# Kernel optimization log

Measured on AMD Instinct MI355X. Metric: run time of the kernel, lower is better.

Reference implementation:

```python
import jax, jax.numpy as jnp
import numpy as np

N = 4096      # num_nodes
B = 32        # batch_size
DIN, DH, DOUT = 64, 128, 32
DIM = 40      # GraphCons embedding dim (hard-coded in source)
ALPHA = 3.0


def setup_inputs() -> dict:
    key = jax.random.key(0)
    ks = jax.random.split(key, 11)
    p = lambda k, shape: (jax.random.normal(k, shape, dtype=jnp.float32) * 0.05)
    return {
        "x": jax.random.normal(ks[0], (B * N, DIN), dtype=jnp.float32),
        "emb1": p(ks[1], (N, DIM)),
        "emb2": p(ks[2], (N, DIM)),
        "lin1_w": p(ks[3], (DIM, DIM)),
        "lin1_b": p(ks[4], (DIM,)),
        "lin2_w": p(ks[5], (DIM, DIM)),
        "lin2_b": p(ks[6], (DIM,)),
        "gcn1_w": p(ks[7], (DIN, DH)),
        "gcn1_b": p(ks[8], (DH,)),
        "gcn2_w": p(ks[9], (DH, DOUT)),
        "gcn2_b": p(ks[10], (DOUT,)),
    }


def reference(x, emb1, emb2, lin1_w, lin1_b, lin2_w, lin2_b,
              gcn1_w, gcn1_b, gcn2_w, gcn2_b):
    # --- GraphCons: learned adjacency. idx = arange(N) so emb(idx) == table.
    n1 = jnp.tanh(ALPHA * (emb1 @ lin1_w + lin1_b))          # [N, DIM]
    n2 = jnp.tanh(ALPHA * (emb2 @ lin2_w + lin2_b))          # [N, DIM]
    a = n1 @ n2.T - n2 @ n1.T                                # [N, N] antisymmetric
    adj = jax.nn.relu(jnp.tanh(ALPHA * a))
    # k == N, so topk/scatter mask is all-ones: adjacency structure = nonzero(adj).
    A = (adj > 0).astype(jnp.float32)                        # binary, zero diagonal
    M = A + jnp.eye(N, dtype=jnp.float32)                    # add self-loops
    # GCN symmetric norm: deg over destination (column) nodes.
    dinv = jax.lax.rsqrt(jnp.sum(M, axis=0))                 # [N], deg >= 1
    Ahat = M * (dinv[:, None] * dinv[None, :])               # [N, N]
    # Batched block-diagonal graph: B independent copies sharing Ahat.
    xb = x.astype(jnp.float32).reshape(B, N, DIN)
    # out[j] = sum_i Ahat[i, j] * (X W)[i]  -> contract over source i
    h = jnp.einsum('ij,bif->bjf', Ahat, xb @ gcn1_w) + gcn1_b  # [B, N, DH]
    h = jax.nn.relu(h)
    h = jnp.einsum('ij,bif->bjf', Ahat, h @ gcn2_w) + gcn2_b   # [B, N, DOUT]
    out = jax.nn.softmax(h, axis=-1)
    return out.reshape(B * N, DOUT)
```

## Files before the change

kernel.cpp:

```cpp
#include <hip/hip_runtime.h>

typedef float f32x4 __attribute__((ext_vector_type(4)));
typedef short s16x8 __attribute__((ext_vector_type(8)));
typedef short s16x4 __attribute__((ext_vector_type(4)));
typedef int i32x4 __attribute__((ext_vector_type(4)));

#define NN 4096
#define NB 32
#define DIN 64
#define DH 128
#define DOUT 32
#define DIM 40
#define KADJ 512

__device__ __forceinline__ unsigned short f2bf(float f) {
    unsigned int u = __float_as_uint(f);
    unsigned int r = (u + 0x7FFFu + ((u >> 16) & 1u)) >> 16;
    return (unsigned short)r;
}
__device__ __forceinline__ float bf2f(unsigned short h) {
    return __uint_as_float(((unsigned int)h) << 16);
}
__device__ __forceinline__ void gload16(const void* g, void* l) {
    __builtin_amdgcn_global_load_lds(
        (const __attribute__((address_space(1))) unsigned int*)g,
        (__attribute__((address_space(3))) unsigned int*)l, 16, 0, 0);
}
__device__ __forceinline__ void bar() {
    asm volatile("" ::: "memory");
    __builtin_amdgcn_s_barrier();
    asm volatile("" ::: "memory");
}

__global__ __launch_bounds__(256) void k_embuv(
    const float* __restrict__ emb1, const float* __restrict__ emb2,
    const float* __restrict__ l1w, const float* __restrict__ l1b,
    const float* __restrict__ l2w, const float* __restrict__ l2b,
    unsigned short* __restrict__ Ux, unsigned short* __restrict__ Vx,
    int* __restrict__ deg)
{
    __shared__ float e1s[16 * DIM], e2s[16 * DIM];
    __shared__ float w1s[DIM * DIM], w2s[DIM * DIM], b1s[DIM], b2s[DIM];
    __shared__ unsigned short Ul[16][KADJ], Vl[16][KADJ];
    const int tid = threadIdx.x;
    const int node0 = blockIdx.x * 16;
    if (tid < 16) deg[node0 + tid] = 0;
    for (int i = tid; i < 16 * DIM; i += 256) {
        e1s[i] = emb1[node0 * DIM + i];
        e2s[i] = emb2[node0 * DIM + i];
    }
    for (int i = tid; i < DIM * DIM; i += 256) { w1s[i] = l1w[i]; w2s[i] = l2w[i]; }
    if (tid < DIM) { b1s[tid] = l1b[tid]; b2s[tid] = l2b[tid]; }
    __syncthreads();
    const int r = tid >> 4;
    const int k0 = (tid & 15) * 5;
    const int PMAP[6] = {0, 0, 1, 1, 0, 2};
    const int QMAP[6] = {0, 1, 0, 1, 2, 0};
    #pragma unroll
    for (int e = 0; e < 5; e++) {
        int k = k0 + e;
        int kp = (k < DIM) ? k : k - DIM;
        float acc1 = b1s[kp], acc2 = b2s[kp];
        for (int kk = 0; kk < DIM; kk++) {
            acc1 += e1s[r * DIM + kk] * w1s[kk * DIM + kp];
            acc2 += e2s[r * DIM + kk] * w2s[kk * DIM + kp];
        }
        float n1v = tanhf(3.0f * acc1), n2v = tanhf(3.0f * acc2);
        float a = (k < DIM) ? n1v : -n2v;
        float b = (k < DIM) ? n2v : n1v;
        unsigned short u0 = f2bf(a); float ra = a - bf2f(u0);
        unsigned short u1 = f2bf(ra); ra -= bf2f(u1);
        unsigned short u2 = f2bf(ra);
        unsigned short v0 = f2bf(b); float rb = b - bf2f(v0);
        unsigned short v1 = f2bf(rb); rb -= bf2f(v1);
        unsigned short v2 = f2bf(rb);
        unsigned short uu[3] = {u0, u1, u2}, vv[3] = {v0, v1, v2};
        #pragma unroll
        for (int bq = 0; bq < 6; bq++) {
            Ul[r][80 * bq + k] = uu[PMAP[bq]];
            Vl[r][80 * bq + k] = vv[QMAP[bq]];
        }
    }
    {
        int c = tid & 15;
        Ul[r][480 + c * 2]     = 0; Vl[r][480 + c * 2]     = 0;
        Ul[r][480 + c * 2 + 1] = 0; Vl[r][480 + c * 2 + 1] = 0;
    }
    __syncthreads();
    #pragma unroll
    for (int q = 0; q < 4; q++) {
        int idx = q * 256 + tid;
        int rr = idx >> 6, c8 = idx & 63;
        size_t off = ((size_t)(node0 + rr)) * KADJ + c8 * 8;
        *(s16x8*)(Ux + off) = *(s16x8*)&Ul[rr][c8 * 8];
        *(s16x8*)(Vx + off) = *(s16x8*)&Vl[rr][c8 * 8];
    }
}

__global__ __launch_bounds__(512, 2) void gemm_adj8(
    const unsigned short* __restrict__ A, const unsigned short* __restrict__ Bt,
    char* __restrict__ Mi8, int* __restrict__ deg)
{
    constexpr int K = KADJ;
    constexpr int NT = K / 64;
    __shared__ __align__(16) unsigned short As[2][256 * 64];
    __shared__ __align__(16) unsigned short Bs[2][256 * 64];

    const int tid = threadIdx.x;
    const int lane = tid & 63;
    const int w = tid >> 6;
    const int wm = w >> 2, wn = w & 3;
    const int fr = lane & 15, kg = lane >> 4;

    const int bid = blockIdx.x;
    const int swz = (bid & 7) * 32 + (bid >> 3);
    const int bx = swz & 15, by = swz >> 4;
    const int c0 = bx * 256, j0 = by * 256;

    const int cid0 = w * 128 + lane, cid1 = cid0 + 64;
    const int r0 = cid0 >> 3, k0c = cid0 & 7;
    const int r1 = cid1 >> 3, k1c = cid1 & 7;
    const int so0 = r0 * K + ((k0c ^ (r0 & 7)) << 3);
    const int so1 = r1 * K + ((k1c ^ (r1 & 7)) << 3);
    const int lb0 = (w * 2 + 0) * 512;
    const int lb1 = (w * 2 + 1) * 512;

    const unsigned short* Aj = A + (size_t)j0 * K;
    const unsigned short* Bc = Bt + (size_t)c0 * K;

#define STAGE_A(buf, half, kt) do { \
    const unsigned short* g_ = Aj + (size_t)((half) * 128) * K + (kt); \
    gload16(g_ + so0, &As[buf][(half) * 8192 + lb0]); \
    gload16(g_ + so1, &As[buf][(half) * 8192 + lb1]); } while (0)
#define STAGE_B(buf, half, kt) do { \
    const unsigned short* g_ = Bc + (size_t)((half) * 128) * K + (kt); \
    gload16(g_ + so0, &Bs[buf][(half) * 8192 + lb0]); \
    gload16(g_ + so1, &Bs[buf][(half) * 8192 + lb1]); } while (0)

    STAGE_A(0, 0, 0);  STAGE_A(0, 1, 0);
    STAGE_B(0, 0, 0);  STAGE_B(0, 1, 0);
    STAGE_A(1, 0, 64); STAGE_A(1, 1, 64);
    STAGE_B(1, 0, 64);
    asm volatile("s_waitcnt vmcnt(6)" ::: "memory");
    bar();

    const int x0 = ((kg) ^ (fr & 7)) << 4;
    const int x1 = ((4 + kg) ^ (fr & 7)) << 4;
    int aOff[8], bOff[4];
    #pragma unroll
    for (int m = 0; m < 8; m++) aOff[m] = (wm * 128 + m * 16 + fr) * 128;
    #pragma unroll
    for (int n = 0; n < 4; n++) bOff[n] = (wn * 64 + n * 16 + fr) * 128;

    s16x8 af0c[4], bf0c[4];
    #pragma unroll
    for (int m = 0; m < 4; m++) af0c[m] = *(const s16x8*)((const char*)As[0] + aOff[m] + x0);
    #pragma unroll
    for (int n = 0; n < 4; n++) bf0c[n] = *(const s16x8*)((const char*)Bs[0] + bOff[n] + x0);

    f32x4 acc[8][4] = {};

    for (int t = 0; t < NT; t++) {
        const int P = t & 1;
        const char* Ap = (const char*)As[P];
        const char* Bp = (const char*)Bs[P];
        const char* Aq = (const char*)As[P ^ 1];
        const char* Bq = (const char*)Bs[P ^ 1];
        const int kt1 = (t + 1) * 64, kt2 = (t + 2) * 64;
        const bool s1 = (t + 1) < NT, s2 = (t + 2) < NT;
        s16x8 af0h[4], af1l[4], af1h[4], bf1[4], af0n[4], bf0n[4];

        #pragma unroll
        for (int m = 0; m < 4; m++) af0h[m] = *(const s16x8*)(Ap + aOff[m + 4] + x0);
        #pragma unroll
        for (int m = 0; m < 4; m++) af1l[m] = *(const s16x8*)(Ap + aOff[m] + x1);
        if (s1) STAGE_B(P ^ 1, 1, kt1);
        __builtin_amdgcn_s_setprio(1);
        #pragma unroll
        for (int m = 0; m < 4; m++)
            #pragma unroll
            for (int n = 0; n < 4; n++)
                acc[m][n] = __builtin_amdgcn_mfma_f32_16x16x32_bf16(af0c[m], bf0c[n], acc[m][n], 0, 0, 0);
        __builtin_amdgcn_s_setprio(0);

        #pragma unroll
        for (int m = 0; m < 4; m++) af1h[m] = *(const s16x8*)(Ap + aOff[m + 4] + x1);
        #pragma unroll
        for (int n = 0; n < 4; n++) bf1[n] = *(const s16x8*)(Bp + bOff[n] + x1);
        __builtin_amdgcn_s_setprio(1);
        #pragma unroll
        for (int m = 4; m < 8; m++)
            #pragma unroll
            for (int n = 0; n < 4; n++)
                acc[m][n] = __builtin_amdgcn_mfma_f32_16x16x32_bf16(af0h[m - 4], bf0c[n], acc[m][n], 0, 0, 0);
        __builtin_amdgcn_s_setprio(0);
        asm volatile("s_waitcnt lgkmcnt(0)" ::: "memory");
        bar();

        __builtin_amdgcn_s_setprio(1);
        #pragma unroll
        for (int m = 0; m < 4; m++)
            #pragma unroll
            for (int n = 0; n < 4; n++)
                acc[m][n] = __builtin_amdgcn_mfma_f32_16x16x32_bf16(af1l[m], bf1[n], acc[m][n], 0, 0, 0);
        __builtin_amdgcn_s_setprio(0);
        if (s2) {
            STAGE_A(P, 0, kt2);
            STAGE_A(P, 1, kt2);
            STAGE_B(P, 0, kt2);
            asm volatile("s_waitcnt vmcnt(6)" ::: "memory");
        } else {
            asm volatile("s_waitcnt vmcnt(0)" ::: "memory");
        }
        bar();

        if (s1) {
            #pragma unroll
            for (int m = 0; m < 4; m++) af0n[m] = *(const s16x8*)(Aq + aOff[m] + x0);
            #pragma unroll
            for (int n = 0; n < 4; n++) bf0n[n] = *(const s16x8*)(Bq + bOff[n] + x0);
        }
        __builtin_amdgcn_s_setprio(1);
        #pragma unroll
        for (int m = 4; m < 8; m++)
            #pragma unroll
            for (int n = 0; n < 4; n++)
                acc[m][n] = __builtin_amdgcn_mfma_f32_16x16x32_bf16(af1h[m - 4], bf1[n], acc[m][n], 0, 0, 0);
        __builtin_amdgcn_s_setprio(0);
        if (s1) {
            #pragma unroll
            for (int m = 0; m < 4; m++) af0c[m] = af0n[m];
            #pragma unroll
            for (int n = 0; n < 4; n++) bf0c[n] = bf0n[n];
        }
    }
#undef STAGE_A
#undef STAGE_B

    #pragma unroll
    for (int m = 0; m < 8; m++) {
        int rbase = j0 + wm * 128 + m * 16 + kg * 4;
        #pragma unroll
        for (int r = 0; r < 4; r++) {
            int row = rbase + r;
            int cnt = 0;
            #pragma unroll
            for (int n = 0; n < 4; n++) {
                int col = c0 + wn * 64 + n * 16 + fr;
                bool bit = (acc[m][n][r] > 0.f) || (row == col);
                Mi8[(size_t)row * NN + col] = bit ? (char)1 : (char)0;
                cnt += bit ? 1 : 0;
            }
            cnt += __shfl_xor(cnt, 1);
            cnt += __shfl_xor(cnt, 2);
            cnt += __shfl_xor(cnt, 4);
            cnt += __shfl_xor(cnt, 8);
            if (fr == 0) atomicAdd(&deg[row], cnt);
        }
    }
}

__global__ void k_dinv(const int* __restrict__ deg, float* __restrict__ dinv,
                       unsigned int* __restrict__ smY) {
    int i = blockIdx.x * 256 + threadIdx.x;
    if (i < NN) { dinv[i] = 1.0f / sqrtf((float)deg[i]); smY[i] = 0u; }
}

__global__ __launch_bounds__(256) void k_y1m(
    const float* __restrict__ x, const float* __restrict__ W1,
    const float* __restrict__ dinv, unsigned short* __restrict__ YT,
    unsigned int* __restrict__ smY)
{
    __shared__ __align__(16) unsigned short Xs[128 * 64];
    __shared__ __align__(16) unsigned short Ws[128 * 64];
    const int tid = threadIdx.x;
    const int i0 = blockIdx.x * 128, b = blockIdx.y;

    const float* xg = x + ((size_t)(b * NN + i0)) * DIN;
    #pragma unroll
    for (int q = 0; q < 8; q++) {
        int idx = q * 256 + tid;
        int row = idx >> 4, c4 = idx & 15;
        f32x4 v = *(const f32x4*)(xg + (size_t)row * DIN + c4 * 4);
        s16x4 pk;
        #pragma unroll
        for (int e = 0; e < 4; e++) pk[e] = (short)f2bf(v[e]);
        int chunk = (c4 >> 1) ^ (row & 7);
        *(s16x4*)((char*)Xs + row * 128 + (chunk << 4) + (c4 & 1) * 8) = pk;
    }
    #pragma unroll
    for (int q = 0; q < 8; q++) {
        int idx = q * 256 + tid;
        int k = idx >> 5, f4 = (idx & 31) * 4;
        f32x4 v = ((const f32x4*)W1)[idx];
        #pragma unroll
        for (int e = 0; e < 4; e++) {
            int f = f4 + e;
            int chunk = (k >> 3) ^ (f & 7);
            *(unsigned short*)((char*)Ws + f * 128 + (chunk << 4) + (k & 7) * 2) = f2bf(v[e]);
        }
    }
    __syncthreads();

    const int lane = tid & 63, w = tid >> 6;
    const int wm = w >> 1, wn = w & 1;
    const int fr = lane & 15, kg = lane >> 4;
    f32x4 acc[4][4] = {};
    #pragma unroll
    for (int ks = 0; ks < 2; ks++) {
        int kc = ks * 4 + kg;
        s16x8 af[4], bf[4];
        #pragma unroll
        for (int mt = 0; mt < 4; mt++) {
            int row = wm * 64 + mt * 16 + fr;
            af[mt] = *(const s16x8*)((const char*)Xs + row * 128 + ((kc ^ (row & 7)) << 4));
        }
        #pragma unroll
        for (int nt = 0; nt < 4; nt++) {
            int f = wn * 64 + nt * 16 + fr;
            bf[nt] = *(const s16x8*)((const char*)Ws + f * 128 + ((kc ^ (f & 7)) << 4));
        }
        #pragma unroll
        for (int mt = 0; mt < 4; mt++)
            #pragma unroll
            for (int nt = 0; nt < 4; nt++)
                acc[mt][nt] = __builtin_amdgcn_mfma_f32_16x16x32_bf16(af[mt], bf[nt], acc[mt][nt], 0, 0, 0);
    }
    float am[4] = {0.f, 0.f, 0.f, 0.f};
    #pragma unroll
    for (int mt = 0; mt < 4; mt++) {
        int ibase = i0 + wm * 64 + mt * 16 + kg * 4;
        float dv[4];
        #pragma unroll
        for (int r = 0; r < 4; r++) dv[r] = dinv[ibase + r];
        #pragma unroll
        for (int nt = 0; nt < 4; nt++) {
            int f = wn * 64 + nt * 16 + fr;
            s16x4 pk;
            #pragma unroll
            for (int r = 0; r < 4; r++) {
                float v = acc[mt][nt][r] * dv[r];
                am[nt] = fmaxf(am[nt], fabsf(v));
                pk[r] = (short)f2bf(v);
            }
            *(s16x4*)(YT + (size_t)(b * DH + f) * NN + ibase) = pk;
        }
    }
    #pragma unroll
    for (int nt = 0; nt < 4; nt++) {
        float mv = am[nt];
        mv = fmaxf(mv, __shfl_xor(mv, 16));
        mv = fmaxf(mv, __shfl_xor(mv, 32));
        if (kg == 0)
            atomicMax(&smY[b * DH + wn * 64 + nt * 16 + fr], __float_as_uint(mv));
    }
}

__global__ __launch_bounds__(256) void k_quant(
    const unsigned short* __restrict__ src, const unsigned int* __restrict__ smax,
    char* __restrict__ dst)
{
    const int c = blockIdx.x;
    const float s = __uint_as_float(smax[c]);
    const float inv = s > 0.f ? 127.0f / s : 0.f;
    const unsigned short* row = src + (size_t)c * NN;
    char* orow = dst + (size_t)c * NN;
    const int base = threadIdx.x * 16;
    s16x8 a = *(const s16x8*)(row + base);
    s16x8 b = *(const s16x8*)(row + base + 8);
    union { char c8[16]; i32x4 v; } u;
    #pragma unroll
    for (int e = 0; e < 8; e++) {
        int q = (int)rintf(bf2f((unsigned short)a[e]) * inv);
        q = q > 127 ? 127 : (q < -127 ? -127 : q);
        u.c8[e] = (char)q;
    }
    #pragma unroll
    for (int e = 0; e < 8; e++) {
        int q = (int)rintf(bf2f((unsigned short)b[e]) * inv);
        q = q > 127 ? 127 : (q < -127 ? -127 : q);
        u.c8[8 + e] = (char)q;
    }
    *(i32x4*)(orow + base) = u.v;
}

__global__ __launch_bounds__(512, 2) void gemm8qi(
    const char* __restrict__ A, const char* __restrict__ Bt,
    unsigned short* __restrict__ H, const float* __restrict__ dinv,
    const unsigned int* __restrict__ smY, const float* __restrict__ bias)
{
    constexpr int KB = NN;
    constexpr int NT = 32;
    __shared__ __align__(16) char As[2][256 * 128];
    __shared__ __align__(16) char Bs[2][256 * 128];

    const int tid = threadIdx.x;
    const int lane = tid & 63;
    const int w = tid >> 6;
    const int wm = w >> 2, wn = w & 3;
    const int fr = lane & 15, kg = lane >> 4;

    const int bid = blockIdx.x;
    const int swz = (bid & 7) * 32 + (bid >> 3);
    const int bx = swz & 15, by = swz >> 4;
    const int c0 = bx * 256, j0 = by * 256;

    const char* Aj = A + (size_t)j0 * KB;
    const char* Bc = Bt + (size_t)c0 * KB;

    const int lr = tid >> 3, kcs = tid & 7;

#define STAGE_AQ(buf, q, kt) do { \
    int ra_ = (q) * 64 + lr; \
    int rb_ = ra_ + 128; \
    gload16(Aj + (size_t)ra_ * KB + (kt) + ((kcs ^ (ra_ & 7)) << 4), \
            &As[buf][(q) * 8192 + tid * 16]); \
    gload16(Aj + (size_t)rb_ * KB + (kt) + ((kcs ^ (rb_ & 7)) << 4), \
            &As[buf][(q) * 8192 + 16384 + tid * 16]); \
} while (0)
#define STAGE_BQ(buf, nh, kt) do { \
    int ca_ = tid, cb_ = tid + 512; \
    int r0_ = (ca_ >> 8) * 64 + (nh) * 32 + ((ca_ >> 3) & 31); \
    int r1_ = (cb_ >> 8) * 64 + (nh) * 32 + ((cb_ >> 3) & 31); \
    gload16(Bc + (size_t)r0_ * KB + (kt) + (((ca_ & 7) ^ (r0_ & 7)) << 4), \
            &Bs[buf][(ca_ >> 8) * 8192 + (nh) * 4096 + (ca_ & 255) * 16]); \
    gload16(Bc + (size_t)r1_ * KB + (kt) + (((cb_ & 7) ^ (r1_ & 7)) << 4), \
            &Bs[buf][(cb_ >> 8) * 8192 + (nh) * 4096 + (cb_ & 255) * 16]); \
} while (0)

    STAGE_AQ(0, 0, 0); STAGE_AQ(0, 1, 0);
    STAGE_BQ(0, 0, 0); STAGE_BQ(0, 1, 0);
    STAGE_BQ(1, 0, 128); STAGE_BQ(1, 1, 128);
    asm volatile("s_waitcnt vmcnt(4)" ::: "memory");
    bar();

    const int x0 = ((kg) ^ (fr & 7)) << 4;
    const int x1 = ((4 + kg) ^ (fr & 7)) << 4;
    int aOff[8], bOff[4];
    #pragma unroll
    for (int m = 0; m < 8; m++) aOff[m] = (wm * 128 + m * 16 + fr) * 128;
    #pragma unroll
    for (int n = 0; n < 4; n++) bOff[n] = (wn * 64 + n * 16 + fr) * 128;

    i32x4 acc[8][4] = {};
    const char* A0p = (const char*)As[0];
    const char* B0p = (const char*)Bs[0];
    const char* A1p = (const char*)As[1];
    const char* B1p = (const char*)Bs[1];

#define MFMA_Q(MB, NB_, AF0, AF1, BK0, BK1) do { \
    __builtin_amdgcn_s_setprio(1); \
    _Pragma("unroll") \
    for (int m = 0; m < 4; m++) { \
        _Pragma("unroll") \
        for (int n = 0; n < 2; n++) { \
            acc[(MB) + m][(NB_) + n] = __builtin_amdgcn_mfma_i32_16x16x64_i8( \
                AF0[m], BK0[n], acc[(MB) + m][(NB_) + n], 0, 0, 0); \
            acc[(MB) + m][(NB_) + n] = __builtin_amdgcn_mfma_i32_16x16x64_i8( \
                AF1[m], BK1[n], acc[(MB) + m][(NB_) + n], 0, 0, 0); \
        } \
    } \
    __builtin_amdgcn_s_setprio(0); \
} while (0)

    i32x4 af0[4], af1[4], b0k0[2], b0k1[2], b1k0[2], b1k1[2];

    for (int T = 0; T < NT; T += 2) {
        const bool s2 = (T + 2) < NT, s3 = (T + 3) < NT;
        const int kt1 = (T + 1) * 128, kt2 = (T + 2) * 128, kt3 = (T + 3) * 128;

        #pragma unroll
        for (int m = 0; m < 4; m++) { af0[m] = *(const i32x4*)(A0p + aOff[m] + x0);
                                      af1[m] = *(const i32x4*)(A0p + aOff[m] + x1); }
        #pragma unroll
        for (int n = 0; n < 2; n++) { b0k0[n] = *(const i32x4*)(B0p + bOff[n] + x0);
                                      b0k1[n] = *(const i32x4*)(B0p + bOff[n] + x1); }
        STAGE_AQ(1, 0, kt1);
        bar();
        MFMA_Q(0, 0, af0, af1, b0k0, b0k1);
        bar();

        #pragma unroll
        for (int n = 0; n < 2; n++) { b1k0[n] = *(const i32x4*)(B0p + bOff[n + 2] + x0);
                                      b1k1[n] = *(const i32x4*)(B0p + bOff[n + 2] + x1); }
        STAGE_AQ(1, 1, kt1);
        bar();
        MFMA_Q(0, 2, af0, af1, b1k0, b1k1);
        bar();

        #pragma unroll
        for (int m = 0; m < 4; m++) { af0[m] = *(const i32x4*)(A0p + aOff[m + 4] + x0);
                                      af1[m] = *(const i32x4*)(A0p + aOff[m + 4] + x1); }
        if (s2) STAGE_BQ(0, 0, kt2);
        bar();
        MFMA_Q(4, 0, af0, af1, b0k0, b0k1);
        bar();

        if (s2) { STAGE_BQ(0, 1, kt2);
                  asm volatile("s_waitcnt vmcnt(4)" ::: "memory"); }
        else    { asm volatile("s_waitcnt vmcnt(0)" ::: "memory"); }
        bar();
        MFMA_Q(4, 2, af0, af1, b1k0, b1k1);
        bar();

        #pragma unroll
        for (int m = 0; m < 4; m++) { af0[m] = *(const i32x4*)(A1p + aOff[m] + x0);
                                      af1[m] = *(const i32x4*)(A1p + aOff[m] + x1); }
        #pragma unroll
        for (int n = 0; n < 2; n++) { b0k0[n] = *(const i32x4*)(B1p + bOff[n] + x0);
                                      b0k1[n] = *(const i32x4*)(B1p + bOff[n] + x1); }
        if (s2) STAGE_AQ(0, 0, kt2);
        bar();
        MFMA_Q(0, 0, af0, af1, b0k0, b0k1);
        bar();

        #pragma unroll
        for (int n = 0; n < 2; n++) { b1k0[n] = *(const i32x4*)(B1p + bOff[n + 2] + x0);
                                      b1k1[n] = *(const i32x4*)(B1p + bOff[n + 2] + x1); }
        if (s2) STAGE_AQ(0, 1, kt2);
        bar();
        MFMA_Q(0, 2, af0, af1, b1k0, b1k1);
        bar();

        #pragma unroll
        for (int m = 0; m < 4; m++) { af0[m] = *(const i32x4*)(A1p + aOff[m + 4] + x0);
                                      af1[m] = *(const i32x4*)(A1p + aOff[m + 4] + x1); }
        if (s3) STAGE_BQ(1, 0, kt3);
        bar();
        MFMA_Q(4, 0, af0, af1, b0k0, b0k1);
        bar();

        if (s3) { STAGE_BQ(1, 1, kt3);
                  asm volatile("s_waitcnt vmcnt(4)" ::: "memory"); }
        else    { asm volatile("s_waitcnt vmcnt(0)" ::: "memory"); }
        bar();
        MFMA_Q(4, 2, af0, af1, b1k0, b1k1);
        bar();
    }
#undef MFMA_Q
#undef STAGE_AQ
#undef STAGE_BQ

    #pragma unroll
    for (int m = 0; m < 8; m++) {
        int rbase = j0 + wm * 128 + m * 16 + kg * 4;
        float dv[4];
        #pragma unroll
        for (int r = 0; r < 4; r++) dv[r] = dinv[rbase + r];
        #pragma unroll
        for (int n = 0; n < 4; n++) {
            int gcol = c0 + wn * 64 + n * 16 + fr;
            float bb = bias[gcol & (DH - 1)];
            float sc = __uint_as_float(smY[gcol]) * (1.0f / 127.0f);
            #pragma unroll
            for (int r = 0; r < 4; r++) {
                float v = (float)acc[m][n][r] * sc * dv[r] + bb;
                v = v > 0.f ? v : 0.f;
                H[(size_t)(rbase + r) * NN + gcol] = f2bf(v);
            }
        }
    }
}

__global__ __launch_bounds__(256) void k_z2(
    const unsigned short* __restrict__ H, const float* __restrict__ W2,
    const float* __restrict__ dinv, unsigned short* __restrict__ ZT)
{
    __shared__ __align__(16) unsigned short Hs[128 * DH];
    __shared__ __align__(16) unsigned short W2Ts[DOUT * DH];
    const int tid = threadIdx.x;
    const int j0 = blockIdx.x * 128, b = blockIdx.y;
    const unsigned short* Hb = H + (size_t)j0 * NN + b * DH;

    #pragma unroll
    for (int q = 0; q < 8; q++) {
        int cid = q * 256 + tid;
        int row = cid >> 4, kc = cid & 15;
        gload16(Hb + (size_t)row * NN + kc * 8, &Hs[cid * 8]);
    }
    #pragma unroll
    for (int q = 0; q < 16; q++) {
        int idx = q * 256 + tid;
        int f = idx >> 5, g = idx & 31;
        W2Ts[g * DH + f] = f2bf(W2[f * DOUT + g]);
    }
    __syncthreads();

    const int lane = tid & 63, w = tid >> 6;
    const int fr = lane & 15, kg = lane >> 4;
    f32x4 acc[2][2] = {};
    #pragma unroll
    for (int ks = 0; ks < 4; ks++) {
        s16x8 af[2], bf[2];
        #pragma unroll
        for (int mt = 0; mt < 2; mt++) {
            int row = w * 32 + mt * 16 + fr;
            af[mt] = *(const s16x8*)&Hs[row * DH + ks * 32 + kg * 8];
        }
        #pragma unroll
        for (int nt = 0; nt < 2; nt++) {
            int g = nt * 16 + fr;
            bf[nt] = *(const s16x8*)&W2Ts[g * DH + ks * 32 + kg * 8];
        }
        #pragma unroll
        for (int mt = 0; mt < 2; mt++)
            #pragma unroll
            for (int nt = 0; nt < 2; nt++)
                acc[mt][nt] = __builtin_amdgcn_mfma_f32_16x16x32_bf16(af[mt], bf[nt], acc[mt][nt], 0, 0, 0);
    }
    #pragma unroll
    for (int mt = 0; mt < 2; mt++) {
        int jbase = j0 + w * 32 + mt * 16 + kg * 4;
        float dv[4];
        #pragma unroll
        for (int r = 0; r < 4; r++) dv[r] = dinv[jbase + r];
        #pragma unroll
        for (int nt = 0; nt < 2; nt++) {
            int g = nt * 16 + fr;
            s16x4 pk;
            #pragma unroll
            for (int r = 0; r < 4; r++)
                pk[r] = (short)f2bf(acc[mt][nt][r] * dv[r]);
            *(s16x4*)(ZT + (size_t)(b * DOUT + g) * NN + jbase) = pk;
        }
    }
}

__global__ __launch_bounds__(256) void gsm2h(
    const char* __restrict__ Mi8, const unsigned short* __restrict__ Bt,
    float* __restrict__ out, const float* __restrict__ dinv,
    const float* __restrict__ bias)
{
    constexpr int KB = NN;
    constexpr int K = NN;
    constexpr int NT = K / 64;
    __shared__ __align__(16) char AsmI[2][64 * 64];
    __shared__ __align__(16) unsigned short Bsm[2][128 * 64];
    const int tid = threadIdx.x;
    const int lane = tid & 63;
    const int w = tid >> 6;
    const int wm = w >> 1, wn = w & 1;
    const int c0 = blockIdx.x * 128;
    const int j0 = blockIdx.y * 64;
    const int fr = lane & 15, kg = lane >> 4;

    const int rowA = tid >> 2, kcA = tid & 3;
    const int srcA = rowA * KB + ((kcA ^ (rowA & 3)) << 4);
    int srcB[4];
    #pragma unroll
    for (int q = 0; q < 4; q++) {
        int cid = q * 256 + tid;
        int row = cid >> 3, kc = cid & 7;
        srcB[q] = row * K + ((kc ^ (row & 7)) << 3);
    }
    const char* Abase = Mi8 + (size_t)j0 * KB;
    const unsigned short* Bbase = Bt + (size_t)c0 * K;

#define STAGE_T(buf, kt) do { \
    gload16(Abase + (kt) + srcA, &AsmI[buf][tid * 16]); \
    _Pragma("unroll") \
    for (int q = 0; q < 4; q++) \
        gload16(Bbase + (kt) + srcB[q], &Bsm[buf][(q * 256 + tid) * 8]); } while (0)

    STAGE_T(0, 0);
    STAGE_T(1, 64);
    asm volatile("s_waitcnt vmcnt(5)" ::: "memory");
    bar();

    const int x0 = (kg ^ (fr & 7)) << 4;
    const int x1 = ((4 + kg) ^ (fr & 7)) << 4;
    int aRow[2], bOff[4];
    #pragma unroll
    for (int m = 0; m < 2; m++) aRow[m] = wm * 32 + m * 16 + fr;
    #pragma unroll
    for (int n = 0; n < 4; n++) bOff[n] = (wn * 64 + n * 16 + fr) * 128;

#define LOAD_AM(dst, Abuf, m_, ks_) do { \
    int kc_ = (ks_) * 2 + (kg >> 1); \
    const char* p_ = (Abuf) + aRow[m_] * 64 + ((kc_ ^ (aRow[m_] & 3)) << 4) + (kg & 1) * 8; \
    int v0_ = *(const int*)p_; \
    int v1_ = *(const int*)(p_ + 4); \
    _Pragma("unroll") \
    for (int e_ = 0; e_ < 4; e_++) dst[e_]     = ((v0_ >> (8 * e_)) & 0xFF) ? (short)0x3F80 : (short)0; \
    _Pragma("unroll") \
    for (int e_ = 0; e_ < 4; e_++) dst[4 + e_] = ((v1_ >> (8 * e_)) & 0xFF) ? (short)0x3F80 : (short)0; \
} while (0)

    s16x8 afc[2][2], bfc[2][4];
    #pragma unroll
    for (int ks = 0; ks < 2; ks++) {
        int xk = ks ? x1 : x0;
        #pragma unroll
        for (int m = 0; m < 2; m++) LOAD_AM(afc[ks][m], (const char*)AsmI[0], m, ks);
        #pragma unroll
        for (int n = 0; n < 4; n++) bfc[ks][n] = *(const s16x8*)((const char*)Bsm[0] + bOff[n] + xk);
    }
    asm volatile("s_waitcnt lgkmcnt(0)" ::: "memory");
    bar();

    f32x4 acc[2][4] = {};

    for (int t = 0; t < NT; t++) {
        const int P = t & 1;
        const bool s1 = (t + 1) < NT, s2 = (t + 2) < NT;

        if (s2) STAGE_T(P, (t + 2) * 64);
        __builtin_amdgcn_s_setprio(1);
        #pragma unroll
        for (int m = 0; m < 2; m++)
            #pragma unroll
            for (int n = 0; n < 4; n++)
                acc[m][n] = __builtin_amdgcn_mfma_f32_16x16x32_bf16(afc[0][m], bfc[0][n], acc[m][n], 0, 0, 0);
        __builtin_amdgcn_s_setprio(0);
        if (s2) asm volatile("s_waitcnt vmcnt(5)" ::: "memory");
        else    asm volatile("s_waitcnt vmcnt(0)" ::: "memory");
        bar();

        s16x8 afn[2][2], bfn[2][4];
        if (s1) {
            const char* Aq = (const char*)AsmI[P ^ 1];
            const char* Bq = (const char*)Bsm[P ^ 1];
            #pragma unroll
            for (int ks = 0; ks < 2; ks++) {
                int xk = ks ? x1 : x0;
                #pragma unroll
                for (int m = 0; m < 2; m++) LOAD_AM(afn[ks][m], Aq, m, ks);
                #pragma unroll
                for (int n = 0; n < 4; n++) bfn[ks][n] = *(const s16x8*)(Bq + bOff[n] + xk);
            }
        }
        __builtin_amdgcn_s_setprio(1);
        #pragma unroll
        for (int m = 0; m < 2; m++)
            #pragma unroll
            for (int n = 0; n < 4; n++)
                acc[m][n] = __builtin_amdgcn_mfma_f32_16x16x32_bf16(afc[1][m], bfc[1][n], acc[m][n], 0, 0, 0);
        __builtin_amdgcn_s_setprio(0);
        asm volatile("s_waitcnt lgkmcnt(0)" ::: "memory");
        bar();
        if (s1) {
            #pragma unroll
            for (int ks = 0; ks < 2; ks++) {
                #pragma unroll
                for (int m = 0; m < 2; m++) afc[ks][m] = afn[ks][m];
                #pragma unroll
                for (int n = 0; n < 4; n++) bfc[ks][n] = bfn[ks][n];
            }
        }
    }
#undef STAGE_T
#undef LOAD_AM

    const float b_lo = bias[fr], b_hi = bias[fr + 16];
    #pragma unroll
    for (int m = 0; m < 2; m++) {
        int rbase = j0 + wm * 32 + m * 16 + kg * 4;
        float dv[4];
        #pragma unroll
        for (int r = 0; r < 4; r++) dv[r] = dinv[rbase + r];
        #pragma unroll
        for (int np = 0; np < 2; np++) {
            int bg = (c0 >> 5) + wn * 2 + np;
            #pragma unroll
            for (int r = 0; r < 4; r++) {
                int row = rbase + r;
                float v0 = acc[m][np * 2][r]     * dv[r] + b_lo;
                float v1 = acc[m][np * 2 + 1][r] * dv[r] + b_hi;
                float mx = fmaxf(v0, v1);
                #pragma unroll
                for (int d = 8; d; d >>= 1) mx = fmaxf(mx, __shfl_xor(mx, d));
                float e0 = expf(v0 - mx), e1 = expf(v1 - mx);
                float s = e0 + e1;
                #pragma unroll
                for (int d = 8; d; d >>= 1) s += __shfl_xor(s, d);
                float inv = 1.0f / s;
                size_t ob = ((size_t)bg * NN + row) * DOUT;
                out[ob + fr]      = e0 * inv;
                out[ob + fr + 16] = e1 * inv;
            }
        }
    }
}

extern "C" void kernel_launch(void* const* d_in, const int* in_sizes, int n_in,
                              void* d_out, int out_size, void* d_ws, size_t ws_size,
                              hipStream_t stream)
{
    (void)in_sizes; (void)n_in; (void)out_size; (void)ws_size;
    const float* x    = (const float*)d_in[0];
    const float* emb1 = (const float*)d_in[1];
    const float* emb2 = (const float*)d_in[2];
    const float* l1w  = (const float*)d_in[3];
    const float* l1b  = (const float*)d_in[4];
    const float* l2w  = (const float*)d_in[5];
    const float* l2b  = (const float*)d_in[6];
    const float* g1w  = (const float*)d_in[7];
    const float* g1b  = (const float*)d_in[8];
    const float* g2w  = (const float*)d_in[9];
    const float* g2b  = (const float*)d_in[10];
    float* out = (float*)d_out;

    char* w = (char*)d_ws;
    int* deg = (int*)w;                       w += NN * 4;
    float* dinv = (float*)w;                  w += NN * 4;
    unsigned int* smY = (unsigned int*)w;     w += NN * 4;
    char* Mi8 = (char*)w;                     w += (size_t)NN * NN;
    unsigned short* YT = (unsigned short*)w;  w += (size_t)NN * NN * 2;
    char* Yq = (char*)w;                      w += (size_t)NN * NN;
    unsigned short* H  = (unsigned short*)w;  w += (size_t)NN * NN * 2;
    unsigned short* ZT = (unsigned short*)w;  w += (size_t)(NB * DOUT) * NN * 2;
    unsigned short* Ux = YT;
    unsigned short* Vx = YT + (size_t)NN * KADJ;

    k_embuv<<<256, 256, 0, stream>>>(emb1, emb2, l1w, l1b, l2w, l2b, Ux, Vx, deg);
    gemm_adj8<<<256, 512, 0, stream>>>(Vx, Ux, Mi8, deg);
    k_dinv<<<16, 256, 0, stream>>>(deg, dinv, smY);
    k_y1m<<<dim3(32, 32), 256, 0, stream>>>(x, g1w, dinv, YT, smY);
    k_quant<<<NN, 256, 0, stream>>>(YT, smY, Yq);
    gemm8qi<<<256, 512, 0, stream>>>(Mi8, Yq, H, dinv, smY, g1b);
    k_z2<<<dim3(32, 32), 256, 0, stream>>>(H, g2w, dinv, ZT);
    gsm2h<<<dim3(8, 64), 256, 0, stream>>>(Mi8, ZT, out, dinv, g2b);
}
```

Before: 224.6 us.

## Replace bf16 second aggregation GEMM with split int8 hi/lo quantized MFMA

The second propagation GEMM stops expanding the int8 adjacency into bf16 and multiplying with bf16 Z. Z is now quantized per column into two int8 planes (high part plus a scaled residual), and the kernel runs two i8 MFMAs per tile against the raw int8 adjacency, with 128-wide K steps. This removes the per-element byte-to-bf16 expansion and halves the B-operand bytes per plane, in exchange for an extra quantization kernel, an atomic max reduction in k_z2, and double the MFMA count. Accuracy depends on the two-level int8 representation matching bf16 closely enough.

After: 206.0 us. -8.3%, faster.

```diff
diff --git a/kernel.cpp b/kernel.cpp
--- a/kernel.cpp
+++ b/kernel.cpp
@@ -261,9 +261,10 @@
 }
 
 __global__ void k_dinv(const int* __restrict__ deg, float* __restrict__ dinv,
-                       unsigned int* __restrict__ smY) {
+                       unsigned int* __restrict__ smY, unsigned int* __restrict__ smZ) {
     int i = blockIdx.x * 256 + threadIdx.x;
     if (i < NN) { dinv[i] = 1.0f / sqrtf((float)deg[i]); smY[i] = 0u; }
+    if (i < NB * DOUT) smZ[i] = 0u;
 }
 
 __global__ __launch_bounds__(256) void k_y1m(
@@ -382,6 +383,33 @@
         u.c8[8 + e] = (char)q;
     }
     *(i32x4*)(orow + base) = u.v;
+}
+
+__global__ __launch_bounds__(256) void k_quant2(
+    const unsigned short* __restrict__ src, const unsigned int* __restrict__ smax,
+    char* __restrict__ dst)
+{
+    const int c = blockIdx.x;
+    const float s = __uint_as_float(smax[c]);
+    const float inv = s > 0.f ? 127.0f / s : 0.f;
+    const unsigned short* row = src + (size_t)c * NN;
+    char* ohi = dst + (size_t)c * NN;
+    char* olo = dst + (size_t)(NB * DOUT + c) * NN;
+    const int base = threadIdx.x * 16;
+    union { char c8[16]; i32x4 v; } uh, ul;
+    #pragma unroll
+    for (int e = 0; e < 16; e++) {
+        float t = bf2f(row[base + e]) * inv;
+        int qh = (int)rintf(t);
+        qh = qh > 127 ? 127 : (qh < -127 ? -127 : qh);
+        float r = (t - (float)qh) * 127.0f;
+        int ql = (int)rintf(r);
+        ql = ql > 127 ? 127 : (ql < -127 ? -127 : ql);
+        uh.c8[e] = (char)qh;
+        ul.c8[e] = (char)ql;
+    }
+    *(i32x4*)(ohi + base) = uh.v;
+    *(i32x4*)(olo + base) = ul.v;
 }
 
 __global__ __launch_bounds__(512, 2) void gemm8qi(
@@ -564,7 +592,8 @@
 
 __global__ __launch_bounds__(256) void k_z2(
     const unsigned short* __restrict__ H, const float* __restrict__ W2,
-    const float* __restrict__ dinv, unsigned short* __restrict__ ZT)
+    const float* __restrict__ dinv, unsigned short* __restrict__ ZT,
+    unsigned int* __restrict__ smZ)
 {
     __shared__ __align__(16) unsigned short Hs[128 * DH];
     __shared__ __align__(16) unsigned short W2Ts[DOUT * DH];
@@ -608,6 +637,7 @@
             for (int nt = 0; nt < 2; nt++)
                 acc[mt][nt] = __builtin_amdgcn_mfma_f32_16x16x32_bf16(af[mt], bf[nt], acc[mt][nt], 0, 0, 0);
     }
+    float am[2] = {0.f, 0.f};
     #pragma unroll
     for (int mt = 0; mt < 2; mt++) {
         int jbase = j0 + w * 32 + mt * 16 + kg * 4;
@@ -619,23 +649,34 @@
             int g = nt * 16 + fr;
             s16x4 pk;
             #pragma unroll
-            for (int r = 0; r < 4; r++)
-                pk[r] = (short)f2bf(acc[mt][nt][r] * dv[r]);
+            for (int r = 0; r < 4; r++) {
+                float v = acc[mt][nt][r] * dv[r];
+                am[nt] = fmaxf(am[nt], fabsf(v));
+                pk[r] = (short)f2bf(v);
+            }
             *(s16x4*)(ZT + (size_t)(b * DOUT + g) * NN + jbase) = pk;
         }
     }
-}
-
-__global__ __launch_bounds__(256) void gsm2h(
-    const char* __restrict__ Mi8, const unsigned short* __restrict__ Bt,
+    #pragma unroll
+    for (int nt = 0; nt < 2; nt++) {
+        float mv = am[nt];
+        mv = fmaxf(mv, __shfl_xor(mv, 16));
+        mv = fmaxf(mv, __shfl_xor(mv, 32));
+        if (kg == 0)
+            atomicMax(&smZ[b * DOUT + nt * 16 + fr], __float_as_uint(mv));
+    }
+}
+
+__global__ __launch_bounds__(256) void gsm2d(
+    const char* __restrict__ Mi8, const char* __restrict__ Zq,
     float* __restrict__ out, const float* __restrict__ dinv,
-    const float* __restrict__ bias)
+    const unsigned int* __restrict__ smZ, const float* __restrict__ bias)
 {
     constexpr int KB = NN;
-    constexpr int K = NN;
-    constexpr int NT = K / 64;
-    __shared__ __align__(16) char AsmI[2][64 * 64];
-    __shared__ __align__(16) unsigned short Bsm[2][128 * 64];
+    constexpr int NT = 32;
+    __shared__ __align__(16) char Asm[2][64 * 128];
+    __shared__ __align__(16) char Bhi[2][128 * 128];
+    __shared__ __align__(16) char Blo[2][128 * 128];
     const int tid = threadIdx.x;
     const int lane = tid & 63;
     const int w = tid >> 6;
@@ -644,97 +685,108 @@
     const int j0 = blockIdx.y * 64;
     const int fr = lane & 15, kg = lane >> 4;
 
-    const int rowA = tid >> 2, kcA = tid & 3;
-    const int srcA = rowA * KB + ((kcA ^ (rowA & 3)) << 4);
-    int srcB[4];
+    int srcA[2], srcB[4];
+    #pragma unroll
+    for (int q = 0; q < 2; q++) {
+        int cid = q * 256 + tid;
+        int row = cid >> 3, kc = cid & 7;
+        srcA[q] = row * KB + ((kc ^ (row & 7)) << 4);
+    }
     #pragma unroll
     for (int q = 0; q < 4; q++) {
         int cid = q * 256 + tid;
         int row = cid >> 3, kc = cid & 7;
-        srcB[q] = row * K + ((kc ^ (row & 7)) << 3);
+        srcB[q] = row * KB + ((kc ^ (row & 7)) << 4);
     }
     const char* Abase = Mi8 + (size_t)j0 * KB;
-    const unsigned short* Bbase = Bt + (size_t)c0 * K;
+    const char* Bh = Zq + (size_t)c0 * KB;
+    const char* Bl = Zq + (size_t)(NB * DOUT + c0) * KB;
 
 #define STAGE_T(buf, kt) do { \
-    gload16(Abase + (kt) + srcA, &AsmI[buf][tid * 16]); \
+    _Pragma("unroll") \
+    for (int q = 0; q < 2; q++) \
+        gload16(Abase + (kt) + srcA[q], &Asm[buf][(q * 256 + tid) * 16]); \
     _Pragma("unroll") \
     for (int q = 0; q < 4; q++) \
-        gload16(Bbase + (kt) + srcB[q], &Bsm[buf][(q * 256 + tid) * 8]); } while (0)
+        gload16(Bh + (kt) + srcB[q], &Bhi[buf][(q * 256 + tid) * 16]); \
+    _Pragma("unroll") \
+    for (int q = 0; q < 4; q++) \
+        gload16(Bl + (kt) + srcB[q], &Blo[buf][(q * 256 + tid) * 16]); } while (0)
 
     STAGE_T(0, 0);
-    STAGE_T(1, 64);
-    asm volatile("s_waitcnt vmcnt(5)" ::: "memory");
+    STAGE_T(1, 128);
+    asm volatile("s_waitcnt vmcnt(10)" ::: "memory");
     bar();
 
     const int x0 = (kg ^ (fr & 7)) << 4;
     const int x1 = ((4 + kg) ^ (fr & 7)) << 4;
-    int aRow[2], bOff[4];
-    #pragma unroll
-    for (int m = 0; m < 2; m++) aRow[m] = wm * 32 + m * 16 + fr;
+    int aOff[2], bOff[4];
+    #pragma unroll
+    for (int m = 0; m < 2; m++) aOff[m] = (wm * 32 + m * 16 + fr) * 128;
     #pragma unroll
     for (int n = 0; n < 4; n++) bOff[n] = (wn * 64 + n * 16 + fr) * 128;
 
-#define LOAD_AM(dst, Abuf, m_, ks_) do { \
-    int kc_ = (ks_) * 2 + (kg >> 1); \
-    const char* p_ = (Abuf) + aRow[m_] * 64 + ((kc_ ^ (aRow[m_] & 3)) << 4) + (kg & 1) * 8; \
-    int v0_ = *(const int*)p_; \
-    int v1_ = *(const int*)(p_ + 4); \
-    _Pragma("unroll") \
-    for (int e_ = 0; e_ < 4; e_++) dst[e_]     = ((v0_ >> (8 * e_)) & 0xFF) ? (short)0x3F80 : (short)0; \
-    _Pragma("unroll") \
-    for (int e_ = 0; e_ < 4; e_++) dst[4 + e_] = ((v1_ >> (8 * e_)) & 0xFF) ? (short)0x3F80 : (short)0; \
-} while (0)
-
-    s16x8 afc[2][2], bfc[2][4];
+    i32x4 afc[2][2], bhc[2][4], blc[2][4];
     #pragma unroll
     for (int ks = 0; ks < 2; ks++) {
         int xk = ks ? x1 : x0;
         #pragma unroll
-        for (int m = 0; m < 2; m++) LOAD_AM(afc[ks][m], (const char*)AsmI[0], m, ks);
-        #pragma unroll
-        for (int n = 0; n < 4; n++) bfc[ks][n] = *(const s16x8*)((const char*)Bsm[0] + bOff[n] + xk);
+        for (int m = 0; m < 2; m++) afc[ks][m] = *(const i32x4*)((const char*)Asm[0] + aOff[m] + xk);
+        #pragma unroll
+        for (int n = 0; n < 4; n++) {
+            bhc[ks][n] = *(const i32x4*)((const char*)Bhi[0] + bOff[n] + xk);
+            blc[ks][n] = *(const i32x4*)((const char*)Blo[0] + bOff[n] + xk);
+        }
     }
     asm volatile("s_waitcnt lgkmcnt(0)" ::: "memory");
     bar();
 
-    f32x4 acc[2][4] = {};
+    i32x4 ah[2][4] = {};
+    i32x4 al[2][4] = {};
 
     for (int t = 0; t < NT; t++) {
         const int P = t & 1;
         const bool s1 = (t + 1) < NT, s2 = (t + 2) < NT;
 
-        if (s2) STAGE_T(P, (t + 2) * 64);
+        if (s2) STAGE_T(P, (t + 2) * 128);
         __builtin_amdgcn_s_setprio(1);
         #pragma unroll
         for (int m = 0; m < 2; m++)
             #pragma unroll
-            for (int n = 0; n < 4; n++)
-                acc[m][n] = __builtin_amdgcn_mfma_f32_16x16x32_bf16(afc[0][m], bfc[0][n], acc[m][n], 0, 0, 0);
+            for (int n = 0; n < 4; n++) {
+                ah[m][n] = __builtin_amdgcn_mfma_i32_16x16x64_i8(afc[0][m], bhc[0][n], ah[m][n], 0, 0, 0);
+                al[m][n] = __builtin_amdgcn_mfma_i32_16x16x64_i8(afc[0][m], blc[0][n], al[m][n], 0, 0, 0);
+            }
         __builtin_amdgcn_s_setprio(0);
-        if (s2) asm volatile("s_waitcnt vmcnt(5)" ::: "memory");
+        if (s2) asm volatile("s_waitcnt vmcnt(10)" ::: "memory");
         else    asm volatile("s_waitcnt vmcnt(0)" ::: "memory");
         bar();
 
-        s16x8 afn[2][2], bfn[2][4];
+        i32x4 afn[2][2], bhn[2][4], bln[2][4];
         if (s1) {
-            const char* Aq = (const char*)AsmI[P ^ 1];
-            const char* Bq = (const char*)Bsm[P ^ 1];
+            const char* Aq = (const char*)Asm[P ^ 1];
+            const char* Bhq = (const char*)Bhi[P ^ 1];
+            const char* Blq = (const char*)Blo[P ^ 1];
             #pragma unroll
             for (int ks = 0; ks < 2; ks++) {
                 int xk = ks ? x1 : x0;
                 #pragma unroll
-                for (int m = 0; m < 2; m++) LOAD_AM(afn[ks][m], Aq, m, ks);
+                for (int m = 0; m < 2; m++) afn[ks][m] = *(const i32x4*)(Aq + aOff[m] + xk);
                 #pragma unroll
-                for (int n = 0; n < 4; n++) bfn[ks][n] = *(const s16x8*)(Bq + bOff[n] + xk);
+                for (int n = 0; n < 4; n++) {
+                    bhn[ks][n] = *(const i32x4*)(Bhq + bOff[n] + xk);
+                    bln[ks][n] = *(const i32x4*)(Blq + bOff[n] + xk);
+                }
             }
         }
         __builtin_amdgcn_s_setprio(1);
         #pragma unroll
         for (int m = 0; m < 2; m++)
             #pragma unroll
-            for (int n = 0; n < 4; n++)
-                acc[m][n] = __builtin_amdgcn_mfma_f32_16x16x32_bf16(afc[1][m], bfc[1][n], acc[m][n], 0, 0, 0);
+            for (int n = 0; n < 4; n++) {
+                ah[m][n] = __builtin_amdgcn_mfma_i32_16x16x64_i8(afc[1][m], bhc[1][n], ah[m][n], 0, 0, 0);
+                al[m][n] = __builtin_amdgcn_mfma_i32_16x16x64_i8(afc[1][m], blc[1][n], al[m][n], 0, 0, 0);
+            }
         __builtin_amdgcn_s_setprio(0);
         asm volatile("s_waitcnt lgkmcnt(0)" ::: "memory");
         bar();
@@ -744,12 +796,11 @@
                 #pragma unroll
                 for (int m = 0; m < 2; m++) afc[ks][m] = afn[ks][m];
                 #pragma unroll
-                for (int n = 0; n < 4; n++) bfc[ks][n] = bfn[ks][n];
+                for (int n = 0; n < 4; n++) { bhc[ks][n] = bhn[ks][n]; blc[ks][n] = bln[ks][n]; }
             }
         }
     }
 #undef STAGE_T
-#undef LOAD_AM
 
     const float b_lo = bias[fr], b_hi = bias[fr + 16];
     #pragma unroll
@@ -761,11 +812,13 @@
         #pragma unroll
         for (int np = 0; np < 2; np++) {
             int bg = (c0 >> 5) + wn * 2 + np;
+            float sc0 = __uint_as_float(smZ[c0 + wn * 64 + np * 32 + fr])      * (1.0f / 127.0f);
+            float sc1 = __uint_as_float(smZ[c0 + wn * 64 + np * 32 + fr + 16]) * (1.0f / 127.0f);
             #pragma unroll
             for (int r = 0; r < 4; r++) {
                 int row = rbase + r;
-                float v0 = acc[m][np * 2][r]     * dv[r] + b_lo;
-                float v1 = acc[m][np * 2 + 1][r] * dv[r] + b_hi;
+                float v0 = ((float)ah[m][np * 2][r]     + (float)al[m][np * 2][r]     * (1.0f / 127.0f)) * sc0 * dv[r] + b_lo;
+                float v1 = ((float)ah[m][np * 2 + 1][r] + (float)al[m][np * 2 + 1][r] * (1.0f / 127.0f)) * sc1 * dv[r] + b_hi;
                 float mx = fmaxf(v0, v1);
                 #pragma unroll
                 for (int d = 8; d; d >>= 1) mx = fmaxf(mx, __shfl_xor(mx, d));
@@ -804,6 +857,7 @@
     int* deg = (int*)w;                       w += NN * 4;
     float* dinv = (float*)w;                  w += NN * 4;
     unsigned int* smY = (unsigned int*)w;     w += NN * 4;
+    unsigned int* smZ = (unsigned int*)w;     w += NB * DOUT * 4;
     char* Mi8 = (char*)w;                     w += (size_t)NN * NN;
     unsigned short* YT = (unsigned short*)w;  w += (size_t)NN * NN * 2;
     char* Yq = (char*)w;                      w += (size_t)NN * NN;
@@ -811,13 +865,15 @@
     unsigned short* ZT = (unsigned short*)w;  w += (size_t)(NB * DOUT) * NN * 2;
     unsigned short* Ux = YT;
     unsigned short* Vx = YT + (size_t)NN * KADJ;
+    char* ZTq2 = Yq;
 
     k_embuv<<<256, 256, 0, stream>>>(emb1, emb2, l1w, l1b, l2w, l2b, Ux, Vx, deg);
     gemm_adj8<<<256, 512, 0, stream>>>(Vx, Ux, Mi8, deg);
-    k_dinv<<<16, 256, 0, stream>>>(deg, dinv, smY);
+    k_dinv<<<16, 256, 0, stream>>>(deg, dinv, smY, smZ);
     k_y1m<<<dim3(32, 32), 256, 0, stream>>>(x, g1w, dinv, YT, smY);
     k_quant<<<NN, 256, 0, stream>>>(YT, smY, Yq);
     gemm8qi<<<256, 512, 0, stream>>>(Mi8, Yq, H, dinv, smY, g1b);
-    k_z2<<<dim3(32, 32), 256, 0, stream>>>(H, g2w, dinv, ZT);
-    gsm2h<<<dim3(8, 64), 256, 0, stream>>>(Mi8, ZT, out, dinv, g2b);
-}
+    k_z2<<<dim3(32, 32), 256, 0, stream>>>(H, g2w, dinv, ZT, smZ);
+    k_quant2<<<NB * DOUT, 256, 0, stream>>>(ZT, smZ, ZTq2);
+    gsm2d<<<dim3(8, 64), 256, 0, stream>>>(Mi8, ZTq2, out, dinv, smZ, g2b);
+}
```
